# Kernel tuning notes

Hardware: AMD Instinct MI355X
Metric: run time of the kernel (lower is better)

The kernel has to match this reference:

```python
import jax, jax.numpy as jnp
import numpy as np

BATCH, SEQ, DMODEL, DSTATE = 4, 2048, 1024, 16


def _hippo_legs(N):
    # HiPPO-LegS: A[n,k] = -sqrt(2n+1)sqrt(2k+1) for n>k, -(n+1) on diag; B[n]=sqrt(2n+1)
    n = np.arange(N)
    b = np.sqrt(2.0 * n + 1.0)
    A = -np.tril(np.outer(b, b), -1) - np.diag(n + 1.0)
    return A.astype(np.float32), b.astype(np.float32)


def setup_inputs() -> dict:
    key = jax.random.key(0)
    x = jax.random.normal(key, (BATCH, SEQ, DMODEL), dtype=jnp.float32)
    A_c, B_c = _hippo_legs(DSTATE)
    dt = 1.0 / float(SEQ)  # simple Euler discretization of the continuous HiPPO ODE
    A = jnp.eye(DSTATE, dtype=jnp.float32) + dt * jnp.asarray(A_c)
    Bvec = dt * jnp.asarray(B_c)
    return {"x": x, "A": A, "Bvec": Bvec}


def reference(x, A, Bvec):
    # x: (B, L, D); A: (N, N) discrete transition; Bvec: (N,) input map.
    # Selective-scan recurrence per channel: h_t = A h_{t-1} + Bvec * x_t, y_t = <Bvec, h_t>
    B, L, D = x.shape
    N = Bvec.shape[0]

    def step(h, xt):
        # h: (B, D, N), xt: (B, D)
        h = jnp.einsum('mn,bdn->bdm', A, h) + xt[..., None] * Bvec
        y = h @ Bvec  # (B, D)
        return h, y

    h0 = jnp.zeros((B, D, N), dtype=x.dtype)
    _, ys = jax.lax.scan(step, h0, jnp.moveaxis(x, 1, 0))  # ys: (L, B, D)
    return jnp.moveaxis(ys, 0, 1)  # (B, L, D)
```

## Files before the change

### kernel.cpp

```cpp
#include <hip/hip_runtime.h>

#define BATCH  4
#define SEQL   2048
#define DMODEL 1024
#define NST    16
#define CT     64
#define NCH    (SEQL / CT)

#define WS_W     1024
#define WS_KV    2048
#define WS_HIN   4096

__global__ __launch_bounds__(256) void ka_tables_scan(const float* __restrict__ x,
                                                      const float* __restrict__ Ain,
                                                      const float* __restrict__ Bvin,
                                                      float* __restrict__ ws) {
    __shared__ double M[256], Mt[256];
    __shared__ double Vd[64][16];
    __shared__ double Wd[65][16];
    __shared__ double bd[16];
    __shared__ float  Pl[64][16];
    __shared__ float  Ap[256];
    __shared__ __align__(16) float xs[16][68];

    const int t   = threadIdx.x;
    const int blk = blockIdx.x;
    const int b   = blk >> 6;
    const int g   = blk & 63;
    const int d0  = g * 16;

    M[t] = (double)Ain[t];
    if (t < 16) {
        bd[t]    = (double)Bvin[t];
        Vd[0][t] = (double)Bvin[t];
        Wd[0][t] = (double)Bvin[t];
    }
    __syncthreads();

    #pragma unroll
    for (int k = 0; k < 6; ++k) {
        const int cnt = 1 << k;
        const int m   = t & 15;
        for (int dd = t >> 4; dd < cnt; dd += 16) {
            double av = 0.0, aw = 0.0;
            #pragma unroll
            for (int l = 0; l < 16; ++l) {
                av += M[m * 16 + l] * Vd[dd][l];
                aw += Wd[dd][l] * M[l * 16 + m];
            }
            Vd[dd + cnt][m] = av;
            Wd[dd + cnt][m] = aw;
        }
        __syncthreads();
        {
            const int i = t >> 4, jj = t & 15;
            double acc = 0.0;
            #pragma unroll
            for (int l = 0; l < 16; ++l) acc += M[i * 16 + l] * M[l * 16 + jj];
            Mt[t] = acc;
            if (k == 5 && t < 16) {
                double aw = 0.0;
                #pragma unroll
                for (int l = 0; l < 16; ++l) aw += Wd[32][l] * M[l * 16 + t];
                Wd[64][t] = aw;
            }
        }
        __syncthreads();
        M[t] = Mt[t];
        __syncthreads();
    }

    Ap[t] = (float)M[t];
    for (int e = t; e < 1024; e += 256) {
        const int r = e >> 4, mm = e & 15;
        Pl[r][mm] = (float)Vd[63 - r][mm];
        ws[WS_W + e] = (float)Wd[r + 1][mm];
    }
    if (t < 64) {
        double kd = 0.0;
        #pragma unroll
        for (int mm = 0; mm < 16; ++mm) kd += bd[mm] * Vd[t][mm];
        ws[WS_KV + 63 + t] = (float)kd;
    }
    __syncthreads();

    const int ch = t >> 4;
    const int m  = t & 15;
    const int d  = d0 + ch;
    const int laneBase = t & 48;
    const int sigt = t >> 2;
    const int c4   = t & 3;

    float Preg[64];
    #pragma unroll
    for (int sg = 0; sg < 64; ++sg) Preg[sg] = Pl[sg][m];

    float Arow[16];
    #pragma unroll
    for (int k = 0; k < 16; ++k) Arow[k] = Ap[m * 16 + k];

    const float* xb = x + (size_t)(b * SEQL) * DMODEL + d0;
    float* hin = ws + WS_HIN;

    float4 cur = *(const float4*)(xb + (size_t)sigt * DMODEL + c4 * 4);

    float s = 0.0f;
    for (int j = 0; j < NCH; ++j) {
        __syncthreads();
        xs[c4 * 4 + 0][sigt] = cur.x;
        xs[c4 * 4 + 1][sigt] = cur.y;
        xs[c4 * 4 + 2][sigt] = cur.z;
        xs[c4 * 4 + 3][sigt] = cur.w;
        __syncthreads();
        if (j + 1 < NCH)
            cur = *(const float4*)(xb + (size_t)((j + 1) * CT + sigt) * DMODEL + c4 * 4);

        float c = 0.0f;
        #pragma unroll
        for (int sg = 0; sg < 16; ++sg) {
            const float4 xv = *(const float4*)(&xs[ch][sg * 4]);
            c = fmaf(Preg[4 * sg + 0], xv.x, c);
            c = fmaf(Preg[4 * sg + 1], xv.y, c);
            c = fmaf(Preg[4 * sg + 2], xv.z, c);
            c = fmaf(Preg[4 * sg + 3], xv.w, c);
        }

        hin[(((size_t)(b * NCH + j) * DMODEL) + d0) * 16 + t] = s;

        float acc = c;
        #pragma unroll
        for (int k = 0; k < 16; ++k)
            acc = fmaf(Arow[k], __shfl(s, laneBase + k, 64), acc);
        s = acc;
    }
}

template <int TT>
__device__ __forceinline__ void k3_body(const float* __restrict__ xs,
                                        const float* __restrict__ ws,
                                        float* __restrict__ y,
                                        int b, int j, int d, int dl) {
    const float* hinp = ws + WS_HIN + (((size_t)(b * NCH + j) * DMODEL) + d) * 16;
    float4 hv[4];
    #pragma unroll
    for (int q = 0; q < 4; ++q) hv[q] = ((const float4*)hinp)[q];

    float h[16];
    #pragma unroll
    for (int q = 0; q < 4; ++q) {
        h[4 * q]     = hv[q].x; h[4 * q + 1] = hv[q].y;
        h[4 * q + 2] = hv[q].z; h[4 * q + 3] = hv[q].w;
    }

    const float* W = ws + WS_W + TT * 16 * 16;
    float yv[16];
    #pragma unroll
    for (int i = 0; i < 16; ++i) {
        float acc = 0.0f;
        #pragma unroll
        for (int m = 0; m < 16; ++m) acc = fmaf(W[i * 16 + m], h[m], acc);
        yv[i] = acc;
    }

    __syncthreads();

    const float* kv63 = ws + WS_KV + 63;
    #pragma unroll
    for (int ss = 0; ss < (TT + 1) * 16; ++ss) {
        const float xv = xs[ss * 64 + dl];
        #pragma unroll
        for (int i = 0; i < 16; ++i) {
            if (TT * 16 + i >= ss)
                yv[i] = fmaf(kv63[TT * 16 + i - ss], xv, yv[i]);
        }
    }

    float* yp = y + ((size_t)(b * SEQL + j * CT + TT * 16)) * DMODEL + d;
    #pragma unroll
    for (int i = 0; i < 16; ++i) yp[(size_t)i * DMODEL] = yv[i];
}

__global__ __launch_bounds__(256, 8) void k3_output(const float* __restrict__ x,
                                                    const float* __restrict__ ws,
                                                    float* __restrict__ y) {
    __shared__ __align__(16) float xs[CT * 64];
    const int blk  = blockIdx.x;
    const int b    = blk >> 9;
    const int j    = (blk >> 4) & 31;
    const int dblk = blk & 15;
    const int t    = threadIdx.x;
    const int tq   = t >> 6;
    const int dl   = t & 63;
    const int d    = dblk * 64 + dl;

    {
        const float* xp = x + ((size_t)(b * SEQL + j * CT)) * DMODEL + dblk * 64;
        #pragma unroll
        for (int k = 0; k < 4; ++k) {
            const int f     = k * 256 + t;
            const int sigma = f >> 4;
            const int cc    = f & 15;
            *(float4*)(&xs[sigma * 64 + cc * 4]) =
                *(const float4*)(xp + (size_t)sigma * DMODEL + cc * 4);
        }
    }

    switch (tq) {
        case 0: k3_body<0>(xs, ws, y, b, j, d, dl); break;
        case 1: k3_body<1>(xs, ws, y, b, j, d, dl); break;
        case 2: k3_body<2>(xs, ws, y, b, j, d, dl); break;
        default: k3_body<3>(xs, ws, y, b, j, d, dl); break;
    }
}

extern "C" void kernel_launch(void* const* d_in, const int* in_sizes, int n_in,
                              void* d_out, int out_size, void* d_ws, size_t ws_size,
                              hipStream_t stream) {
    (void)in_sizes; (void)n_in; (void)out_size; (void)ws_size;
    const float* x  = (const float*)d_in[0];
    const float* A  = (const float*)d_in[1];
    const float* Bv = (const float*)d_in[2];
    float* out = (float*)d_out;
    float* ws  = (float*)d_ws;

    ka_tables_scan<<<256, 256, 0, stream>>>(x, A, Bv, ws);
    k3_output<<<2048, 256, 0, stream>>>(x, ws, out);
}
```

Baseline: 119.1 us.

## Fuse chunk-state scan and output computation into a single sequential kernel

Merges the two-kernel design (scan writes per-chunk hidden states to workspace, then a second 2048-block kernel computes outputs) into one 256-block kernel. Each block computes its outputs inline during the chunk loop, using register-resident W and kv tables and a cross-lane reduction, with double-buffered LDS for x. This removes the workspace round-trip and the second launch. In exchange, parallelism drops to 256 blocks running a serial loop of 32 chunks with heavy per-iteration work, which may leave the GPU underutilised.

Measured after the change: 136.3 us. +14.4%, slower.

```diff
diff --git a/kernel.cpp b/kernel.cpp
--- a/kernel.cpp
+++ b/kernel.cpp
@@ -3,25 +3,20 @@
 #define BATCH  4
 #define SEQL   2048
 #define DMODEL 1024
-#define NST    16
 #define CT     64
 #define NCH    (SEQL / CT)
 
-#define WS_W     1024
-#define WS_KV    2048
-#define WS_HIN   4096
-
-__global__ __launch_bounds__(256) void ka_tables_scan(const float* __restrict__ x,
-                                                      const float* __restrict__ Ain,
-                                                      const float* __restrict__ Bvin,
-                                                      float* __restrict__ ws) {
-    __shared__ double M[256], Mt[256];
+__global__ __launch_bounds__(256, 1) void fused_all(const float* __restrict__ x,
+                                                    const float* __restrict__ Ain,
+                                                    const float* __restrict__ Bvin,
+                                                    float* __restrict__ y) {
+    __shared__ double Mb[256], Mt[256];
     __shared__ double Vd[64][16];
     __shared__ double Wd[65][16];
     __shared__ double bd[16];
-    __shared__ float  Pl[64][16];
-    __shared__ float  Ap[256];
-    __shared__ __align__(16) float xs[16][68];
+    __shared__ __align__(16) float xsT[2][16][68];
+    __shared__ float sLDS[16][17];
+    __shared__ float kvLDS[128];
 
     const int t   = threadIdx.x;
     const int blk = blockIdx.x;
@@ -29,7 +24,17 @@
     const int g   = blk & 63;
     const int d0  = g * 16;
 
-    M[t] = (double)Ain[t];
+    const int l    = t & 63;
+    const int wv   = t >> 6;
+    const int part = l >> 4;
+    const int chT  = l & 15;
+    const int chS  = t >> 4;
+    const int m    = t & 15;
+    const int sigma = t >> 2;
+    const int c4    = t & 3;
+    const int laneBase = l & 48;
+
+    Mb[t] = (double)Ain[t];
     if (t < 16) {
         bd[t]    = (double)Bvin[t];
         Vd[0][t] = (double)Bvin[t];
@@ -40,189 +45,177 @@
     #pragma unroll
     for (int k = 0; k < 6; ++k) {
         const int cnt = 1 << k;
-        const int m   = t & 15;
+        const int mm  = t & 15;
         for (int dd = t >> 4; dd < cnt; dd += 16) {
             double av = 0.0, aw = 0.0;
             #pragma unroll
-            for (int l = 0; l < 16; ++l) {
-                av += M[m * 16 + l] * Vd[dd][l];
-                aw += Wd[dd][l] * M[l * 16 + m];
+            for (int q = 0; q < 16; ++q) {
+                av += Mb[mm * 16 + q] * Vd[dd][q];
+                aw += Wd[dd][q] * Mb[q * 16 + mm];
             }
-            Vd[dd + cnt][m] = av;
-            Wd[dd + cnt][m] = aw;
+            Vd[dd + cnt][mm] = av;
+            Wd[dd + cnt][mm] = aw;
         }
         __syncthreads();
         {
             const int i = t >> 4, jj = t & 15;
             double acc = 0.0;
             #pragma unroll
-            for (int l = 0; l < 16; ++l) acc += M[i * 16 + l] * M[l * 16 + jj];
+            for (int q = 0; q < 16; ++q) acc += Mb[i * 16 + q] * Mb[q * 16 + jj];
             Mt[t] = acc;
             if (k == 5 && t < 16) {
                 double aw = 0.0;
                 #pragma unroll
-                for (int l = 0; l < 16; ++l) aw += Wd[32][l] * M[l * 16 + t];
+                for (int q = 0; q < 16; ++q) aw += Wd[32][q] * Mb[q * 16 + t];
                 Wd[64][t] = aw;
             }
         }
         __syncthreads();
-        M[t] = Mt[t];
-        __syncthreads();
-    }
-
-    Ap[t] = (float)M[t];
-    for (int e = t; e < 1024; e += 256) {
-        const int r = e >> 4, mm = e & 15;
-        Pl[r][mm] = (float)Vd[63 - r][mm];
-        ws[WS_W + e] = (float)Wd[r + 1][mm];
-    }
+        Mb[t] = Mt[t];
+        __syncthreads();
+    }
+
     if (t < 64) {
         double kd = 0.0;
         #pragma unroll
-        for (int mm = 0; mm < 16; ++mm) kd += bd[mm] * Vd[t][mm];
-        ws[WS_KV + 63 + t] = (float)kd;
+        for (int q = 0; q < 16; ++q) kd += bd[q] * Vd[t][q];
+        kvLDS[63 + t] = (float)kd;
+    } else if (t < 127) {
+        kvLDS[t - 64] = 0.0f;
+    } else {
+        kvLDS[127] = 0.0f;
+    }
+    sLDS[chS][m] = 0.0f;
+
+    const float* xbase = x + (size_t)(b * SEQL) * DMODEL + d0 + 4 * c4;
+    {
+        float4 cur = *(const float4*)(xbase + (size_t)sigma * DMODEL);
+        xsT[0][4 * c4 + 0][sigma] = cur.x;
+        xsT[0][4 * c4 + 1][sigma] = cur.y;
+        xsT[0][4 * c4 + 2][sigma] = cur.z;
+        xsT[0][4 * c4 + 3][sigma] = cur.w;
     }
     __syncthreads();
 
-    const int ch = t >> 4;
-    const int m  = t & 15;
-    const int d  = d0 + ch;
-    const int laneBase = t & 48;
-    const int sigt = t >> 2;
-    const int c4   = t & 3;
-
     float Preg[64];
     #pragma unroll
-    for (int sg = 0; sg < 64; ++sg) Preg[sg] = Pl[sg][m];
+    for (int sg = 0; sg < 64; ++sg) Preg[sg] = (float)Vd[63 - sg][m];
 
     float Arow[16];
     #pragma unroll
-    for (int k = 0; k < 16; ++k) Arow[k] = Ap[m * 16 + k];
-
-    const float* xb = x + (size_t)(b * SEQL) * DMODEL + d0;
-    float* hin = ws + WS_HIN;
-
-    float4 cur = *(const float4*)(xb + (size_t)sigt * DMODEL + c4 * 4);
+    for (int k = 0; k < 16; ++k) Arow[k] = (float)Mb[m * 16 + k];
+
+    float kvs[31];
+    {
+        const int kvbase = 48 + 16 * (wv - part);
+        #pragma unroll
+        for (int u = 0; u < 31; ++u) kvs[u] = kvLDS[kvbase + u];
+    }
+
+    float Wreg[16][4];
+    #pragma unroll
+    for (int i = 0; i < 16; ++i)
+        #pragma unroll
+        for (int mm = 0; mm < 4; ++mm)
+            Wreg[i][mm] = (float)Wd[16 * wv + i + 1][4 * part + mm];
 
     float s = 0.0f;
+    int buf = 0;
     for (int j = 0; j < NCH; ++j) {
-        __syncthreads();
-        xs[c4 * 4 + 0][sigt] = cur.x;
-        xs[c4 * 4 + 1][sigt] = cur.y;
-        xs[c4 * 4 + 2][sigt] = cur.z;
-        xs[c4 * 4 + 3][sigt] = cur.w;
-        __syncthreads();
+        float4 nxt;
         if (j + 1 < NCH)
-            cur = *(const float4*)(xb + (size_t)((j + 1) * CT + sigt) * DMODEL + c4 * 4);
+            nxt = *(const float4*)(xbase + (size_t)((j + 1) * CT + sigma) * DMODEL);
+
+        float xcol[16];
+        #pragma unroll
+        for (int k4 = 0; k4 < 4; ++k4) {
+            const float4 v = *(const float4*)(&xsT[buf][chT][16 * part + 4 * k4]);
+            xcol[4 * k4 + 0] = v.x; xcol[4 * k4 + 1] = v.y;
+            xcol[4 * k4 + 2] = v.z; xcol[4 * k4 + 3] = v.w;
+        }
+        float yv[16];
+        #pragma unroll
+        for (int i = 0; i < 16; ++i) yv[i] = 0.0f;
+        #pragma unroll
+        for (int k = 0; k < 16; ++k)
+            #pragma unroll
+            for (int i = 0; i < 16; ++i)
+                yv[i] = fmaf(kvs[i - k + 15], xcol[k], yv[i]);
+
+        float h4[4];
+        #pragma unroll
+        for (int mm = 0; mm < 4; ++mm) h4[mm] = sLDS[chT][4 * part + mm];
+        #pragma unroll
+        for (int i = 0; i < 16; ++i)
+            #pragma unroll
+            for (int mm = 0; mm < 4; ++mm)
+                yv[i] = fmaf(Wreg[i][mm], h4[mm], yv[i]);
+
+        #pragma unroll
+        for (int i = 0; i < 16; ++i) {
+            yv[i] += __shfl_xor(yv[i], 16, 64);
+            yv[i] += __shfl_xor(yv[i], 32, 64);
+        }
+
+        {
+            float* yp = y + ((size_t)(b * SEQL + j * CT + 16 * wv)) * DMODEL + d0 + chT;
+            switch (part) {
+                case 0:
+                    yp[0 * (size_t)DMODEL]  = yv[0];  yp[1 * (size_t)DMODEL]  = yv[1];
+                    yp[2 * (size_t)DMODEL]  = yv[2];  yp[3 * (size_t)DMODEL]  = yv[3];
+                    break;
+                case 1:
+                    yp[4 * (size_t)DMODEL]  = yv[4];  yp[5 * (size_t)DMODEL]  = yv[5];
+                    yp[6 * (size_t)DMODEL]  = yv[6];  yp[7 * (size_t)DMODEL]  = yv[7];
+                    break;
+                case 2:
+                    yp[8 * (size_t)DMODEL]  = yv[8];  yp[9 * (size_t)DMODEL]  = yv[9];
+                    yp[10 * (size_t)DMODEL] = yv[10]; yp[11 * (size_t)DMODEL] = yv[11];
+                    break;
+                default:
+                    yp[12 * (size_t)DMODEL] = yv[12]; yp[13 * (size_t)DMODEL] = yv[13];
+                    yp[14 * (size_t)DMODEL] = yv[14]; yp[15 * (size_t)DMODEL] = yv[15];
+                    break;
+            }
+        }
 
         float c = 0.0f;
         #pragma unroll
-        for (int sg = 0; sg < 16; ++sg) {
-            const float4 xv = *(const float4*)(&xs[ch][sg * 4]);
-            c = fmaf(Preg[4 * sg + 0], xv.x, c);
-            c = fmaf(Preg[4 * sg + 1], xv.y, c);
-            c = fmaf(Preg[4 * sg + 2], xv.z, c);
-            c = fmaf(Preg[4 * sg + 3], xv.w, c);
-        }
-
-        hin[(((size_t)(b * NCH + j) * DMODEL) + d0) * 16 + t] = s;
-
+        for (int sg4 = 0; sg4 < 16; ++sg4) {
+            const float4 v = *(const float4*)(&xsT[buf][chS][4 * sg4]);
+            c = fmaf(Preg[4 * sg4 + 0], v.x, c);
+            c = fmaf(Preg[4 * sg4 + 1], v.y, c);
+            c = fmaf(Preg[4 * sg4 + 2], v.z, c);
+            c = fmaf(Preg[4 * sg4 + 3], v.w, c);
+        }
         float acc = c;
         #pragma unroll
         for (int k = 0; k < 16; ++k)
             acc = fmaf(Arow[k], __shfl(s, laneBase + k, 64), acc);
+
+        __syncthreads();
+
         s = acc;
-    }
-}
-
-template <int TT>
-__device__ __forceinline__ void k3_body(const float* __restrict__ xs,
-                                        const float* __restrict__ ws,
-                                        float* __restrict__ y,
-                                        int b, int j, int d, int dl) {
-    const float* hinp = ws + WS_HIN + (((size_t)(b * NCH + j) * DMODEL) + d) * 16;
-    float4 hv[4];
-    #pragma unroll
-    for (int q = 0; q < 4; ++q) hv[q] = ((const float4*)hinp)[q];
-
-    float h[16];
-    #pragma unroll
-    for (int q = 0; q < 4; ++q) {
-        h[4 * q]     = hv[q].x; h[4 * q + 1] = hv[q].y;
-        h[4 * q + 2] = hv[q].z; h[4 * q + 3] = hv[q].w;
-    }
-
-    const float* W = ws + WS_W + TT * 16 * 16;
-    float yv[16];
-    #pragma unroll
-    for (int i = 0; i < 16; ++i) {
-        float acc = 0.0f;
-        #pragma unroll
-        for (int m = 0; m < 16; ++m) acc = fmaf(W[i * 16 + m], h[m], acc);
-        yv[i] = acc;
-    }
-
-    __syncthreads();
-
-    const float* kv63 = ws + WS_KV + 63;
-    #pragma unroll
-    for (int ss = 0; ss < (TT + 1) * 16; ++ss) {
-        const float xv = xs[ss * 64 + dl];
-        #pragma unroll
-        for (int i = 0; i < 16; ++i) {
-            if (TT * 16 + i >= ss)
-                yv[i] = fmaf(kv63[TT * 16 + i - ss], xv, yv[i]);
-        }
-    }
-
-    float* yp = y + ((size_t)(b * SEQL + j * CT + TT * 16)) * DMODEL + d;
-    #pragma unroll
-    for (int i = 0; i < 16; ++i) yp[(size_t)i * DMODEL] = yv[i];
-}
-
-__global__ __launch_bounds__(256, 8) void k3_output(const float* __restrict__ x,
-                                                    const float* __restrict__ ws,
-                                                    float* __restrict__ y) {
-    __shared__ __align__(16) float xs[CT * 64];
-    const int blk  = blockIdx.x;
-    const int b    = blk >> 9;
-    const int j    = (blk >> 4) & 31;
-    const int dblk = blk & 15;
-    const int t    = threadIdx.x;
-    const int tq   = t >> 6;
-    const int dl   = t & 63;
-    const int d    = dblk * 64 + dl;
-
-    {
-        const float* xp = x + ((size_t)(b * SEQL + j * CT)) * DMODEL + dblk * 64;
-        #pragma unroll
-        for (int k = 0; k < 4; ++k) {
-            const int f     = k * 256 + t;
-            const int sigma = f >> 4;
-            const int cc    = f & 15;
-            *(float4*)(&xs[sigma * 64 + cc * 4]) =
-                *(const float4*)(xp + (size_t)sigma * DMODEL + cc * 4);
-        }
-    }
-
-    switch (tq) {
-        case 0: k3_body<0>(xs, ws, y, b, j, d, dl); break;
-        case 1: k3_body<1>(xs, ws, y, b, j, d, dl); break;
-        case 2: k3_body<2>(xs, ws, y, b, j, d, dl); break;
-        default: k3_body<3>(xs, ws, y, b, j, d, dl); break;
+        sLDS[chS][m] = s;
+        if (j + 1 < NCH) {
+            xsT[buf ^ 1][4 * c4 + 0][sigma] = nxt.x;
+            xsT[buf ^ 1][4 * c4 + 1][sigma] = nxt.y;
+            xsT[buf ^ 1][4 * c4 + 2][sigma] = nxt.z;
+            xsT[buf ^ 1][4 * c4 + 3][sigma] = nxt.w;
+        }
+        __syncthreads();
+        buf ^= 1;
     }
 }
 
 extern "C" void kernel_launch(void* const* d_in, const int* in_sizes, int n_in,
                               void* d_out, int out_size, void* d_ws, size_t ws_size,
                               hipStream_t stream) {
-    (void)in_sizes; (void)n_in; (void)out_size; (void)ws_size;
+    (void)in_sizes; (void)n_in; (void)out_size; (void)d_ws; (void)ws_size;
     const float* x  = (const float*)d_in[0];
     const float* A  = (const float*)d_in[1];
     const float* Bv = (const float*)d_in[2];
     float* out = (float*)d_out;
-    float* ws  = (float*)d_ws;
-
-    ka_tables_scan<<<256, 256, 0, stream>>>(x, A, Bv, ws);
-    k3_output<<<2048, 256, 0, stream>>>(x, ws, out);
+
+    fused_all<<<256, 256, 0, stream>>>(x, A, Bv, out);
 }
```

## Double-buffer x staging in chunk scan and split dependent FMA chains

Applied to the files above, without the earlier changes.

The sequential chunk scan now keeps two shared-memory buffers for x. Each iteration fills the buffer for the next chunk while reading the current one, so only one barrier per iteration is needed instead of two, and the global prefetch runs two chunks ahead. The long serial FMA chains in the chunk contraction and the state update are split into several independent accumulators to shorten dependency latency, which changes the floating-point summation order slightly. The output kernel's launch bounds minimum-blocks hint is lowered from 8 to 4, which gives the compiler more register room at possible cost to occupancy.

New measurement: 118.2 us. About the same (-0.8%).

```diff
diff --git a/kernel.cpp b/kernel.cpp
--- a/kernel.cpp
+++ b/kernel.cpp
@@ -3,7 +3,6 @@
 #define BATCH  4
 #define SEQL   2048
 #define DMODEL 1024
-#define NST    16
 #define CT     64
 #define NCH    (SEQL / CT)
 
@@ -21,7 +20,7 @@
     __shared__ double bd[16];
     __shared__ float  Pl[64][16];
     __shared__ float  Ap[256];
-    __shared__ __align__(16) float xs[16][68];
+    __shared__ __align__(16) float xsT[2][16][68];
 
     const int t   = threadIdx.x;
     const int blk = blockIdx.x;
@@ -40,16 +39,16 @@
     #pragma unroll
     for (int k = 0; k < 6; ++k) {
         const int cnt = 1 << k;
-        const int m   = t & 15;
+        const int mm  = t & 15;
         for (int dd = t >> 4; dd < cnt; dd += 16) {
             double av = 0.0, aw = 0.0;
             #pragma unroll
             for (int l = 0; l < 16; ++l) {
-                av += M[m * 16 + l] * Vd[dd][l];
-                aw += Wd[dd][l] * M[l * 16 + m];
+                av += M[mm * 16 + l] * Vd[dd][l];
+                aw += Wd[dd][l] * M[l * 16 + mm];
             }
-            Vd[dd + cnt][m] = av;
-            Wd[dd + cnt][m] = aw;
+            Vd[dd + cnt][mm] = av;
+            Wd[dd + cnt][mm] = aw;
         }
         __syncthreads();
         {
@@ -82,14 +81,25 @@
         for (int mm = 0; mm < 16; ++mm) kd += bd[mm] * Vd[t][mm];
         ws[WS_KV + 63 + t] = (float)kd;
     }
-    __syncthreads();
 
     const int ch = t >> 4;
     const int m  = t & 15;
-    const int d  = d0 + ch;
     const int laneBase = t & 48;
-    const int sigt = t >> 2;
-    const int c4   = t & 3;
+    const int sigma = t >> 2;
+    const int c4    = t & 3;
+
+    const float* xb2 = x + (size_t)(b * SEQL) * DMODEL + d0 + 4 * c4;
+    float* hin = ws + WS_HIN;
+
+    {
+        float4 v0 = *(const float4*)(xb2 + (size_t)sigma * DMODEL);
+        xsT[0][4 * c4 + 0][sigma] = v0.x;
+        xsT[0][4 * c4 + 1][sigma] = v0.y;
+        xsT[0][4 * c4 + 2][sigma] = v0.z;
+        xsT[0][4 * c4 + 3][sigma] = v0.w;
+    }
+    float4 cur = *(const float4*)(xb2 + (size_t)(CT + sigma) * DMODEL);
+    __syncthreads();
 
     float Preg[64];
     #pragma unroll
@@ -99,39 +109,53 @@
     #pragma unroll
     for (int k = 0; k < 16; ++k) Arow[k] = Ap[m * 16 + k];
 
-    const float* xb = x + (size_t)(b * SEQL) * DMODEL + d0;
-    float* hin = ws + WS_HIN;
-
-    float4 cur = *(const float4*)(xb + (size_t)sigt * DMODEL + c4 * 4);
-
     float s = 0.0f;
+    int buf = 0;
     for (int j = 0; j < NCH; ++j) {
-        __syncthreads();
-        xs[c4 * 4 + 0][sigt] = cur.x;
-        xs[c4 * 4 + 1][sigt] = cur.y;
-        xs[c4 * 4 + 2][sigt] = cur.z;
-        xs[c4 * 4 + 3][sigt] = cur.w;
-        __syncthreads();
-        if (j + 1 < NCH)
-            cur = *(const float4*)(xb + (size_t)((j + 1) * CT + sigt) * DMODEL + c4 * 4);
-
-        float c = 0.0f;
-        #pragma unroll
-        for (int sg = 0; sg < 16; ++sg) {
-            const float4 xv = *(const float4*)(&xs[ch][sg * 4]);
-            c = fmaf(Preg[4 * sg + 0], xv.x, c);
-            c = fmaf(Preg[4 * sg + 1], xv.y, c);
-            c = fmaf(Preg[4 * sg + 2], xv.z, c);
-            c = fmaf(Preg[4 * sg + 3], xv.w, c);
-        }
+        float4 nxt = cur;
+        if (j + 2 < NCH)
+            nxt = *(const float4*)(xb2 + (size_t)((j + 2) * CT + sigma) * DMODEL);
+
+        if (j + 1 < NCH) {
+            xsT[buf ^ 1][4 * c4 + 0][sigma] = cur.x;
+            xsT[buf ^ 1][4 * c4 + 1][sigma] = cur.y;
+            xsT[buf ^ 1][4 * c4 + 2][sigma] = cur.z;
+            xsT[buf ^ 1][4 * c4 + 3][sigma] = cur.w;
+        }
+
+        float a0 = 0.0f, a1 = 0.0f, a2 = 0.0f, a3 = 0.0f;
+        #pragma unroll
+        for (int r = 0; r < 4; ++r) {
+            const int o = 16 * r;
+            const float4 q0 = *(const float4*)(&xsT[buf][ch][o + 0]);
+            const float4 q1 = *(const float4*)(&xsT[buf][ch][o + 4]);
+            const float4 q2 = *(const float4*)(&xsT[buf][ch][o + 8]);
+            const float4 q3 = *(const float4*)(&xsT[buf][ch][o + 12]);
+            a0 = fmaf(Preg[o + 0], q0.x, a0);  a0 = fmaf(Preg[o + 1], q0.y, a0);
+            a0 = fmaf(Preg[o + 2], q0.z, a0);  a0 = fmaf(Preg[o + 3], q0.w, a0);
+            a1 = fmaf(Preg[o + 4], q1.x, a1);  a1 = fmaf(Preg[o + 5], q1.y, a1);
+            a1 = fmaf(Preg[o + 6], q1.z, a1);  a1 = fmaf(Preg[o + 7], q1.w, a1);
+            a2 = fmaf(Preg[o + 8], q2.x, a2);  a2 = fmaf(Preg[o + 9], q2.y, a2);
+            a2 = fmaf(Preg[o + 10], q2.z, a2); a2 = fmaf(Preg[o + 11], q2.w, a2);
+            a3 = fmaf(Preg[o + 12], q3.x, a3); a3 = fmaf(Preg[o + 13], q3.y, a3);
+            a3 = fmaf(Preg[o + 14], q3.z, a3); a3 = fmaf(Preg[o + 15], q3.w, a3);
+        }
+        const float c = (a0 + a1) + (a2 + a3);
 
         hin[(((size_t)(b * NCH + j) * DMODEL) + d0) * 16 + t] = s;
 
-        float acc = c;
-        #pragma unroll
-        for (int k = 0; k < 16; ++k)
-            acc = fmaf(Arow[k], __shfl(s, laneBase + k, 64), acc);
-        s = acc;
+        float u0 = 0.0f, u1 = 0.0f;
+        #pragma unroll
+        for (int k = 0; k < 8; ++k) {
+            u0 = fmaf(Arow[k],     __shfl(s, laneBase + k, 64),     u0);
+            u1 = fmaf(Arow[k + 8], __shfl(s, laneBase + k + 8, 64), u1);
+        }
+        const float snew = c + (u0 + u1);
+
+        __syncthreads();
+        s = snew;
+        cur = nxt;
+        buf ^= 1;
     }
 }
 
@@ -180,7 +204,7 @@
     for (int i = 0; i < 16; ++i) yp[(size_t)i * DMODEL] = yv[i];
 }
 
-__global__ __launch_bounds__(256, 8) void k3_output(const float* __restrict__ x,
+__global__ __launch_bounds__(256, 4) void k3_output(const float* __restrict__ x,
                                                     const float* __restrict__ ws,
                                                     float* __restrict__ y) {
     __shared__ __align__(16) float xs[CT * 64];
```

## Split chunk-state computation from sequential carry scan into separate parallel kernels

Applied to the files above, without the earlier changes.

The fused kernel that both computed per-chunk input contributions and ran the serial inter-chunk carry is split in two. The first kernel computes all chunk states in parallel across 512 blocks, one channel per thread, and writes them to a workspace buffer. A light second kernel then runs only the 32-step carry recurrence over those states. This shortens the serial critical path and uses more blocks in the heavy phase, at the cost of an extra launch and a round trip through global memory for the chunk states. The launch bound on the output kernel is also lowered from 8 to 4 blocks.

Measured after the change: 120.8 us. Within noise of the previous version (+1.4%).

```diff
diff --git a/kernel.cpp b/kernel.cpp
--- a/kernel.cpp
+++ b/kernel.cpp
@@ -3,31 +3,37 @@
 #define BATCH  4
 #define SEQL   2048
 #define DMODEL 1024
-#define NST    16
 #define CT     64
 #define NCH    (SEQL / CT)
 
 #define WS_W     1024
 #define WS_KV    2048
+#define WS_APOW  2176
 #define WS_HIN   4096
-
-__global__ __launch_bounds__(256) void ka_tables_scan(const float* __restrict__ x,
-                                                      const float* __restrict__ Ain,
-                                                      const float* __restrict__ Bvin,
-                                                      float* __restrict__ ws) {
+#define WS_CBUF  (WS_HIN + BATCH * NCH * DMODEL * 16)
+
+__global__ __launch_bounds__(256) void k1_tables_chunkstate(const float* __restrict__ x,
+                                                            const float* __restrict__ Ain,
+                                                            const float* __restrict__ Bvin,
+                                                            float* __restrict__ ws) {
     __shared__ double M[256], Mt[256];
     __shared__ double Vd[64][16];
     __shared__ double Wd[65][16];
     __shared__ double bd[16];
-    __shared__ float  Pl[64][16];
-    __shared__ float  Ap[256];
-    __shared__ __align__(16) float xs[16][68];
-
-    const int t   = threadIdx.x;
-    const int blk = blockIdx.x;
-    const int b   = blk >> 6;
-    const int g   = blk & 63;
-    const int d0  = g * 16;
+    __shared__ __align__(16) float Pl[64][16];
+
+    const int t    = threadIdx.x;
+    const int blk  = blockIdx.x;
+    const int b    = blk >> 7;
+    const int j    = (blk >> 2) & 31;
+    const int dblk = blk & 3;
+    const int d    = dblk * 256 + t;
+
+    const float* xp = x + ((size_t)(b * SEQL + j * CT)) * DMODEL + d;
+
+    float xa[8], xb[8];
+    #pragma unroll
+    for (int s = 0; s < 8; ++s) xa[s] = xp[(size_t)s * DMODEL];
 
     M[t] = (double)Ain[t];
     if (t < 16) {
@@ -40,16 +46,16 @@
     #pragma unroll
     for (int k = 0; k < 6; ++k) {
         const int cnt = 1 << k;
-        const int m   = t & 15;
+        const int mm  = t & 15;
         for (int dd = t >> 4; dd < cnt; dd += 16) {
             double av = 0.0, aw = 0.0;
             #pragma unroll
             for (int l = 0; l < 16; ++l) {
-                av += M[m * 16 + l] * Vd[dd][l];
-                aw += Wd[dd][l] * M[l * 16 + m];
+                av += M[mm * 16 + l] * Vd[dd][l];
+                aw += Wd[dd][l] * M[l * 16 + mm];
             }
-            Vd[dd + cnt][m] = av;
-            Wd[dd + cnt][m] = aw;
+            Vd[dd + cnt][mm] = av;
+            Wd[dd + cnt][mm] = aw;
         }
         __syncthreads();
         {
@@ -70,64 +76,87 @@
         __syncthreads();
     }
 
-    Ap[t] = (float)M[t];
     for (int e = t; e < 1024; e += 256) {
         const int r = e >> 4, mm = e & 15;
         Pl[r][mm] = (float)Vd[63 - r][mm];
         ws[WS_W + e] = (float)Wd[r + 1][mm];
     }
+    ws[WS_APOW + t] = (float)M[t];
     if (t < 64) {
         double kd = 0.0;
         #pragma unroll
-        for (int mm = 0; mm < 16; ++mm) kd += bd[mm] * Vd[t][mm];
+        for (int q = 0; q < 16; ++q) kd += bd[q] * Vd[t][q];
         ws[WS_KV + 63 + t] = (float)kd;
     }
     __syncthreads();
 
-    const int ch = t >> 4;
-    const int m  = t & 15;
-    const int d  = d0 + ch;
+    float c[16];
+    #pragma unroll
+    for (int m = 0; m < 16; ++m) c[m] = 0.0f;
+
+    #pragma unroll
+    for (int g = 0; g < 8; ++g) {
+        float* cur = (g & 1) ? xb : xa;
+        float* nxt = (g & 1) ? xa : xb;
+        if (g < 7) {
+            #pragma unroll
+            for (int s = 0; s < 8; ++s)
+                nxt[s] = xp[(size_t)((g + 1) * 8 + s) * DMODEL];
+        }
+        #pragma unroll
+        for (int s = 0; s < 8; ++s) {
+            const int ss = g * 8 + s;
+            const float xv = cur[s];
+            const float4 p0 = *(const float4*)(&Pl[ss][0]);
+            const float4 p1 = *(const float4*)(&Pl[ss][4]);
+            const float4 p2 = *(const float4*)(&Pl[ss][8]);
+            const float4 p3 = *(const float4*)(&Pl[ss][12]);
+            c[0]  = fmaf(p0.x, xv, c[0]);  c[1]  = fmaf(p0.y, xv, c[1]);
+            c[2]  = fmaf(p0.z, xv, c[2]);  c[3]  = fmaf(p0.w, xv, c[3]);
+            c[4]  = fmaf(p1.x, xv, c[4]);  c[5]  = fmaf(p1.y, xv, c[5]);
+            c[6]  = fmaf(p1.z, xv, c[6]);  c[7]  = fmaf(p1.w, xv, c[7]);
+            c[8]  = fmaf(p2.x, xv, c[8]);  c[9]  = fmaf(p2.y, xv, c[9]);
+            c[10] = fmaf(p2.z, xv, c[10]); c[11] = fmaf(p2.w, xv, c[11]);
+            c[12] = fmaf(p3.x, xv, c[12]); c[13] = fmaf(p3.y, xv, c[13]);
+            c[14] = fmaf(p3.z, xv, c[14]); c[15] = fmaf(p3.w, xv, c[15]);
+        }
+    }
+
+    float4* outp = (float4*)(ws + WS_CBUF + (((size_t)(b * NCH + j) * DMODEL) + d) * 16);
+    #pragma unroll
+    for (int q = 0; q < 4; ++q)
+        outp[q] = make_float4(c[4 * q], c[4 * q + 1], c[4 * q + 2], c[4 * q + 3]);
+}
+
+__global__ __launch_bounds__(256) void k2_carry(float* __restrict__ ws) {
+    const int blk = blockIdx.x;
+    const int b   = blk >> 6;
+    const int d0  = (blk & 63) * 16;
+    const int t   = threadIdx.x;
+    const int m   = t & 15;
+    const int ch  = t >> 4;
+    const int d   = d0 + ch;
     const int laneBase = t & 48;
-    const int sigt = t >> 2;
-    const int c4   = t & 3;
-
-    float Preg[64];
-    #pragma unroll
-    for (int sg = 0; sg < 64; ++sg) Preg[sg] = Pl[sg][m];
+
+    const float* cbuf    = ws + WS_CBUF;
+    const size_t base0   = (((size_t)(b * NCH) * DMODEL) + d) * 16 + m;
+    const size_t jstride = (size_t)DMODEL * 16;
+
+    float cpre[NCH];
+    #pragma unroll
+    for (int j = 0; j < NCH; ++j)
+        cpre[j] = cbuf[base0 + (size_t)j * jstride];
 
     float Arow[16];
     #pragma unroll
-    for (int k = 0; k < 16; ++k) Arow[k] = Ap[m * 16 + k];
-
-    const float* xb = x + (size_t)(b * SEQL) * DMODEL + d0;
+    for (int k = 0; k < 16; ++k) Arow[k] = ws[WS_APOW + m * 16 + k];
+
     float* hin = ws + WS_HIN;
-
-    float4 cur = *(const float4*)(xb + (size_t)sigt * DMODEL + c4 * 4);
-
     float s = 0.0f;
+    #pragma unroll
     for (int j = 0; j < NCH; ++j) {
-        __syncthreads();
-        xs[c4 * 4 + 0][sigt] = cur.x;
-        xs[c4 * 4 + 1][sigt] = cur.y;
-        xs[c4 * 4 + 2][sigt] = cur.z;
-        xs[c4 * 4 + 3][sigt] = cur.w;
-        __syncthreads();
-        if (j + 1 < NCH)
-            cur = *(const float4*)(xb + (size_t)((j + 1) * CT + sigt) * DMODEL + c4 * 4);
-
-        float c = 0.0f;
-        #pragma unroll
-        for (int sg = 0; sg < 16; ++sg) {
-            const float4 xv = *(const float4*)(&xs[ch][sg * 4]);
-            c = fmaf(Preg[4 * sg + 0], xv.x, c);
-            c = fmaf(Preg[4 * sg + 1], xv.y, c);
-            c = fmaf(Preg[4 * sg + 2], xv.z, c);
-            c = fmaf(Preg[4 * sg + 3], xv.w, c);
-        }
-
-        hin[(((size_t)(b * NCH + j) * DMODEL) + d0) * 16 + t] = s;
-
-        float acc = c;
+        hin[base0 + (size_t)j * jstride] = s;
+        float acc = cpre[j];
         #pragma unroll
         for (int k = 0; k < 16; ++k)
             acc = fmaf(Arow[k], __shfl(s, laneBase + k, 64), acc);
@@ -180,7 +209,7 @@
     for (int i = 0; i < 16; ++i) yp[(size_t)i * DMODEL] = yv[i];
 }
 
-__global__ __launch_bounds__(256, 8) void k3_output(const float* __restrict__ x,
+__global__ __launch_bounds__(256, 4) void k3_output(const float* __restrict__ x,
                                                     const float* __restrict__ ws,
                                                     float* __restrict__ y) {
     __shared__ __align__(16) float xs[CT * 64];
@@ -223,6 +252,7 @@
     float* out = (float*)d_out;
     float* ws  = (float*)d_ws;
 
-    ka_tables_scan<<<256, 256, 0, stream>>>(x, A, Bv, ws);
+    k1_tables_chunkstate<<<512, 256, 0, stream>>>(x, A, Bv, ws);
+    k2_carry<<<256, 256, 0, stream>>>(ws);
     k3_output<<<2048, 256, 0, stream>>>(x, ws, out);
 }
```
